# Kernel tuning notes

Measured on AMD Instinct MI355X. Metric: run time of the kernel, lower is better.

The kernel has to match this reference:

```python
import jax, jax.numpy as jnp
import numpy as np

EYE_PENALTY = 1.0e6


def setup_inputs() -> dict:
    key = jax.random.key(0)
    k1, k2 = jax.random.split(key)
    B, NIN, NK, DK = 512, 1024, 128, 5
    x = jax.random.normal(k1, (B, NIN), dtype=jnp.float32)
    theta = jax.random.normal(k2, (NIN, NK, DK), dtype=jnp.float32) * 0.05
    log_weight_scale = jnp.zeros((NK, DK), dtype=jnp.float32)
    bias = jnp.full((NK,), -1.0, dtype=jnp.float32)
    return {"x": x, "theta": theta, "log_weight_scale": log_weight_scale, "bias": bias}


def reference(x, theta, log_weight_scale, bias):
    # kernel = theta * exp(log_weight_scale) / ||theta||_2 (norm over input dim)
    l2 = jnp.sqrt(jnp.sum(theta * theta, axis=0))            # [K, D]
    kernel = theta * (jnp.exp(log_weight_scale) / l2)[None]   # [NIN, K, D]
    actv = jnp.einsum('bi,ikd->bkd', x, kernel)               # [B, K, D]
    B = x.shape[0]
    # all-pairs L1 distance per kernel: [B, K, B]
    diff = actv[:, :, :, None] - jnp.transpose(actv, (1, 2, 0))[None]  # [B,K,D,B]
    abs_dif = jnp.sum(jnp.abs(diff), axis=2)                  # [B, K, B]
    abs_dif = abs_dif + EYE_PENALTY * jnp.eye(B, dtype=x.dtype)[:, None, :]
    f = jnp.sum(jnp.exp(-abs_dif), axis=2) + bias[None, :]    # [B, K]
    return jnp.concatenate([x, f], axis=1)                    # [B, NIN + K]
```

## Files before the change

### kernel.cpp

```cpp
#include <hip/hip_runtime.h>
#include <hip/hip_fp16.h>
#include <math.h>

constexpr int B    = 512;
constexpr int NIN  = 1024;
constexpr int NK   = 128;
constexpr int DK   = 5;
constexpr int NF   = NK * DK;
constexpr int NOUT = NIN + NK;
constexpr int SPLITK = 8;
constexpr int LDA = 136;
#define LOG2E 1.44269504088896f

typedef _Float16 f16x2 __attribute__((ext_vector_type(2)));
typedef _Float16 f16x4 __attribute__((ext_vector_type(4)));
typedef _Float16 f16x8 __attribute__((ext_vector_type(8)));
typedef float    f32x4 __attribute__((ext_vector_type(4)));

union H2 { __half2 h; f16x2 v; unsigned u; };

__global__ __launch_bounds__(256) void gemm_kernel(
        const float* __restrict__ x,
        const float* __restrict__ theta,
        __half* __restrict__ actvP16,
        float* __restrict__ ps) {
    __shared__ _Float16 Ath[64 * LDA];
    __shared__ _Float16 Bxh[64 * LDA];
    __shared__ float    red2[16][64];

    const int t    = threadIdx.x;
    const int tile = blockIdx.x >> 3;
    const int z    = blockIdx.x & 7;
    const int n0   = (tile >> 3) * 64;
    const int b0   = (tile & 7) * 64;
    const bool do_ps = (tile & 7) == 0;
    const int kw   = z * 128;

    const int kq  = t >> 4;
    const int tn4 = (t & 15) * 4;
    float4 tv[8];
    #pragma unroll
    for (int i = 0; i < 8; ++i)
        tv[i] = *(const float4*)&theta[(kw + kq * 8 + i) * NF + n0 + tn4];

    const int br = t >> 2;
    const int ki = t & 3;
    float4 xv[8];
    #pragma unroll
    for (int i = 0; i < 8; ++i)
        xv[i] = *(const float4*)&x[(b0 + br) * NIN + kw + (ki + i * 4) * 4];

    if (do_ps) {
        float sq0 = 0.f, sq1 = 0.f, sq2 = 0.f, sq3 = 0.f;
        #pragma unroll
        for (int i = 0; i < 8; ++i) {
            sq0 += tv[i].x * tv[i].x;  sq1 += tv[i].y * tv[i].y;
            sq2 += tv[i].z * tv[i].z;  sq3 += tv[i].w * tv[i].w;
        }
        red2[kq][tn4 + 0] = sq0;  red2[kq][tn4 + 1] = sq1;
        red2[kq][tn4 + 2] = sq2;  red2[kq][tn4 + 3] = sq3;
    }

    {
        f16x8 h;
        #pragma unroll
        for (int i = 0; i < 8; ++i) h[i] = (_Float16)tv[i].x;
        *(f16x8*)&Ath[(tn4 + 0) * LDA + kq * 8] = h;
        #pragma unroll
        for (int i = 0; i < 8; ++i) h[i] = (_Float16)tv[i].y;
        *(f16x8*)&Ath[(tn4 + 1) * LDA + kq * 8] = h;
        #pragma unroll
        for (int i = 0; i < 8; ++i) h[i] = (_Float16)tv[i].z;
        *(f16x8*)&Ath[(tn4 + 2) * LDA + kq * 8] = h;
        #pragma unroll
        for (int i = 0; i < 8; ++i) h[i] = (_Float16)tv[i].w;
        *(f16x8*)&Ath[(tn4 + 3) * LDA + kq * 8] = h;
    }
    #pragma unroll
    for (int i = 0; i < 8; ++i) {
        f16x4 h;
        h[0] = (_Float16)xv[i].x;  h[1] = (_Float16)xv[i].y;
        h[2] = (_Float16)xv[i].z;  h[3] = (_Float16)xv[i].w;
        *(f16x4*)&Bxh[br * LDA + (ki + i * 4) * 4] = h;
    }
    __syncthreads();

    const int w   = t >> 6;
    const int l   = t & 63;
    const int r16 = l & 15;
    const int kg  = l >> 4;

    f32x4 acc0 = {0.f,0.f,0.f,0.f}, acc1 = {0.f,0.f,0.f,0.f};
    f32x4 acc2 = {0.f,0.f,0.f,0.f}, acc3 = {0.f,0.f,0.f,0.f};
    #pragma unroll
    for (int ks = 0; ks < 4; ++ks) {
        const f16x8 av  = *(const f16x8*)&Ath[(w*16 + r16)*LDA + ks*32 + kg*8];
        const f16x8 bv0 = *(const f16x8*)&Bxh[( 0 + r16)*LDA + ks*32 + kg*8];
        const f16x8 bv1 = *(const f16x8*)&Bxh[(16 + r16)*LDA + ks*32 + kg*8];
        const f16x8 bv2 = *(const f16x8*)&Bxh[(32 + r16)*LDA + ks*32 + kg*8];
        const f16x8 bv3 = *(const f16x8*)&Bxh[(48 + r16)*LDA + ks*32 + kg*8];
        acc0 = __builtin_amdgcn_mfma_f32_16x16x32_f16(av, bv0, acc0, 0, 0, 0);
        acc1 = __builtin_amdgcn_mfma_f32_16x16x32_f16(av, bv1, acc1, 0, 0, 0);
        acc2 = __builtin_amdgcn_mfma_f32_16x16x32_f16(av, bv2, acc2, 0, 0, 0);
        acc3 = __builtin_amdgcn_mfma_f32_16x16x32_f16(av, bv3, acc3, 0, 0, 0);
    }

    {
        __half* dst = actvP16 + (size_t)z * NF * B
                    + (size_t)(n0 + w*16 + kg*4) * B + b0 + r16;
        #pragma unroll
        for (int j = 0; j < 4; ++j) {
            dst[j*B +  0] = __float2half(acc0[j]);
            dst[j*B + 16] = __float2half(acc1[j]);
            dst[j*B + 32] = __float2half(acc2[j]);
            dst[j*B + 48] = __float2half(acc3[j]);
        }
    }
    if (do_ps) {
        __syncthreads();
        if (t < 64) {
            float tot = 0.f;
            #pragma unroll
            for (int rr = 0; rr < 16; ++rr) tot += red2[rr][t];
            ps[z * NF + n0 + t] = tot;
        }
    }
}

__global__ __launch_bounds__(256) void pairwise_kernel(
        const __half* __restrict__ actvP16,
        const float* __restrict__ ps,
        const float* __restrict__ lws,
        const float* __restrict__ bias,
        const float* __restrict__ x,
        float* __restrict__ out) {
    __shared__ __half a16s[DK * B];
    __shared__ float  red[8 * 64];
    __shared__ float  s_sh[DK];
    __shared__ float  red_ps[DK * SPLITK];

    const int k = blockIdx.x;
    const int e = blockIdx.y;
    const int t = threadIdx.x;

    if (e < 4) {
        const int row = k * 4 + e;
        ((float4*)out)[row * (NOUT/4) + t] = ((const float4*)x)[row * (NIN/4) + t];
    }

    if (t < DK * SPLITK)
        red_ps[t] = ps[(t / DK) * NF + k * DK + (t % DK)];

    const size_t slab = (size_t)k * DK * B;
    float acc0f[8], acc1f[8];
    {
        #pragma unroll
        for (int i = 0; i < 8; ++i) { acc0f[i] = 0.f; acc1f[i] = 0.f; }
        #pragma unroll
        for (int z = 0; z < SPLITK; ++z) {
            const f16x8 v = *(const f16x8*)(actvP16 + (size_t)z * NF * B + slab + t * 8);
            #pragma unroll
            for (int i = 0; i < 8; ++i) acc0f[i] += (float)v[i];
        }
        if (t < 64) {
            #pragma unroll
            for (int z = 0; z < SPLITK; ++z) {
                const f16x8 v = *(const f16x8*)(actvP16 + (size_t)z * NF * B + slab + 2048 + t * 8);
                #pragma unroll
                for (int i = 0; i < 8; ++i) acc1f[i] += (float)v[i];
            }
        }
    }
    __syncthreads();
    if (t < DK) {
        float sum = 0.f;
        #pragma unroll
        for (int c = 0; c < SPLITK; ++c) sum += red_ps[c * DK + t];
        s_sh[t] = __expf(lws[k * DK + t]) * rsqrtf(sum) * LOG2E;
    }
    __syncthreads();
    {
        const float s0 = s_sh[t >> 6];
        f16x8 h;
        #pragma unroll
        for (int i = 0; i < 8; ++i) h[i] = (_Float16)(acc0f[i] * s0);
        *(f16x8*)&a16s[t * 8] = h;
        if (t < 64) {
            const float s1 = s_sh[4];
            #pragma unroll
            for (int i = 0; i < 8; ++i) h[i] = (_Float16)(acc1f[i] * s1);
            *(f16x8*)&a16s[2048 + t * 8] = h;
        }
    }
    __syncthreads();

    const int g  = t >> 5;
    const int r  = t & 31;
    const int ba = e * 64 + r;
    const int bb = ba + 32;

    __half2 A2[DK], B2[DK];
    #pragma unroll
    for (int d = 0; d < DK; ++d) {
        A2[d] = __half2half2(a16s[d * B + ba]);
        B2[d] = __half2half2(a16s[d * B + bb]);
    }
    const H2 ones = {__half2half2(__float2half(1.0f))};

    float accA = 0.f, accB = 0.f;
    const int bp0 = g * 64;

    union W8 { f16x8 v; __half2 h[4]; };
    #pragma unroll 2
    for (int m = 0; m < 8; ++m) {
        const int bp = bp0 + m * 8;
        W8 w0, w1, w2, w3, w4;
        w0.v = *(const f16x8*)&a16s[0*B + bp];
        w1.v = *(const f16x8*)&a16s[1*B + bp];
        w2.v = *(const f16x8*)&a16s[2*B + bp];
        w3.v = *(const f16x8*)&a16s[3*B + bp];
        w4.v = *(const f16x8*)&a16s[4*B + bp];
        #pragma unroll
        for (int c = 0; c < 4; ++c) {
            __half2 dA = __habs2(__hsub2(A2[0], w0.h[c]));
            dA = __hadd2(dA, __habs2(__hsub2(A2[1], w1.h[c])));
            dA = __hadd2(dA, __habs2(__hsub2(A2[2], w2.h[c])));
            dA = __hadd2(dA, __habs2(__hsub2(A2[3], w3.h[c])));
            dA = __hadd2(dA, __habs2(__hsub2(A2[4], w4.h[c])));
            H2 eA; eA.h = h2exp2(__hneg2(dA));
            __half2 dB = __habs2(__hsub2(B2[0], w0.h[c]));
            dB = __hadd2(dB, __habs2(__hsub2(B2[1], w1.h[c])));
            dB = __hadd2(dB, __habs2(__hsub2(B2[2], w2.h[c])));
            dB = __hadd2(dB, __habs2(__hsub2(B2[3], w3.h[c])));
            dB = __hadd2(dB, __habs2(__hsub2(B2[4], w4.h[c])));
            H2 eB; eB.h = h2exp2(__hneg2(dB));
#if __has_builtin(__builtin_amdgcn_fdot2)
            accA = __builtin_amdgcn_fdot2(eA.v, ones.v, accA, false);
            accB = __builtin_amdgcn_fdot2(eB.v, ones.v, accB, false);
#else
            accA += __low2float(eA.h) + __high2float(eA.h);
            accB += __low2float(eB.h) + __high2float(eB.h);
#endif
        }
    }
    red[g * 64 + r]      = accA;
    red[g * 64 + 32 + r] = accB;
    __syncthreads();
    if (t < 64) {
        float f = -1.0f + bias[k];
        #pragma unroll
        for (int gg = 0; gg < 8; ++gg) f += red[gg * 64 + t];
        out[(e * 64 + t) * NOUT + NIN + k] = f;
    }
}

extern "C" void kernel_launch(void* const* d_in, const int* in_sizes, int n_in,
                              void* d_out, int out_size, void* d_ws, size_t ws_size,
                              hipStream_t stream) {
    const float* x     = (const float*)d_in[0];
    const float* theta = (const float*)d_in[1];
    const float* lws   = (const float*)d_in[2];
    const float* bias  = (const float*)d_in[3];
    float* out = (float*)d_out;

    char* wsb = (char*)d_ws;
    float*  ps       = (float*)wsb;
    __half* actvP16  = (__half*)(wsb + (64 << 10));

    gemm_kernel<<<dim3(640), 256, 0, stream>>>(x, theta, actvP16, ps);
    pairwise_kernel<<<dim3(NK, 8), 256, 0, stream>>>(actvP16, ps, lws, bias, x, out);
}
```

Before: 24.82 us.

## Halve GEMM N-tile to double blocks; widen pairwise blocks to 512 threads

The GEMM now uses 32-wide feature tiles instead of 64, so it launches twice as many blocks with fewer MFMAs and less theta staging per block. This aims to fill more CUs. The pairwise kernel moves to 512-thread blocks covering 128 query rows, over a grid of NK x 4. Separate thread ranges handle the x copy, the ps load and the split-K reduction, so each slab of activations is reduced and rescaled by half as many blocks. In exchange, the redundant x loads per GEMM block double, and each pairwise block carries more per-block serial work.

```diff
diff --git a/kernel.cpp b/kernel.cpp
--- a/kernel.cpp
+++ b/kernel.cpp
@@ -12,36 +12,37 @@
 constexpr int LDA = 136;
 #define LOG2E 1.44269504088896f
 
-typedef _Float16 f16x2 __attribute__((ext_vector_type(2)));
 typedef _Float16 f16x4 __attribute__((ext_vector_type(4)));
 typedef _Float16 f16x8 __attribute__((ext_vector_type(8)));
 typedef float    f32x4 __attribute__((ext_vector_type(4)));
 
-union H2 { __half2 h; f16x2 v; unsigned u; };
+union H2 { __half2 h; unsigned u; };
 
 __global__ __launch_bounds__(256) void gemm_kernel(
         const float* __restrict__ x,
         const float* __restrict__ theta,
         __half* __restrict__ actvP16,
         float* __restrict__ ps) {
-    __shared__ _Float16 Ath[64 * LDA];
+    __shared__ _Float16 Ath[32 * LDA];
     __shared__ _Float16 Bxh[64 * LDA];
-    __shared__ float    red2[16][64];
+    __shared__ float    red2[32][33];
 
     const int t    = threadIdx.x;
     const int tile = blockIdx.x >> 3;
     const int z    = blockIdx.x & 7;
-    const int n0   = (tile >> 3) * 64;
-    const int b0   = (tile & 7) * 64;
-    const bool do_ps = (tile & 7) == 0;
+    const int nt   = tile >> 3;
+    const int bt   = tile & 7;
+    const int n0   = nt * 32;
+    const int b0   = bt * 64;
+    const bool do_ps = (bt == 0);
     const int kw   = z * 128;
 
-    const int kq  = t >> 4;
-    const int tn4 = (t & 15) * 4;
-    float4 tv[8];
-    #pragma unroll
-    for (int i = 0; i < 8; ++i)
-        tv[i] = *(const float4*)&theta[(kw + kq * 8 + i) * NF + n0 + tn4];
+    const int kq = t >> 3;
+    const int nc = (t & 7) * 4;
+    float4 tv0 = *(const float4*)&theta[(kw + kq*4 + 0) * NF + n0 + nc];
+    float4 tv1 = *(const float4*)&theta[(kw + kq*4 + 1) * NF + n0 + nc];
+    float4 tv2 = *(const float4*)&theta[(kw + kq*4 + 2) * NF + n0 + nc];
+    float4 tv3 = *(const float4*)&theta[(kw + kq*4 + 3) * NF + n0 + nc];
 
     const int br = t >> 2;
     const int ki = t & 3;
@@ -51,30 +52,22 @@
         xv[i] = *(const float4*)&x[(b0 + br) * NIN + kw + (ki + i * 4) * 4];
 
     if (do_ps) {
-        float sq0 = 0.f, sq1 = 0.f, sq2 = 0.f, sq3 = 0.f;
-        #pragma unroll
-        for (int i = 0; i < 8; ++i) {
-            sq0 += tv[i].x * tv[i].x;  sq1 += tv[i].y * tv[i].y;
-            sq2 += tv[i].z * tv[i].z;  sq3 += tv[i].w * tv[i].w;
-        }
-        red2[kq][tn4 + 0] = sq0;  red2[kq][tn4 + 1] = sq1;
-        red2[kq][tn4 + 2] = sq2;  red2[kq][tn4 + 3] = sq3;
+        red2[kq][nc + 0] = tv0.x*tv0.x + tv1.x*tv1.x + tv2.x*tv2.x + tv3.x*tv3.x;
+        red2[kq][nc + 1] = tv0.y*tv0.y + tv1.y*tv1.y + tv2.y*tv2.y + tv3.y*tv3.y;
+        red2[kq][nc + 2] = tv0.z*tv0.z + tv1.z*tv1.z + tv2.z*tv2.z + tv3.z*tv3.z;
+        red2[kq][nc + 3] = tv0.w*tv0.w + tv1.w*tv1.w + tv2.w*tv2.w + tv3.w*tv3.w;
     }
 
     {
-        f16x8 h;
-        #pragma unroll
-        for (int i = 0; i < 8; ++i) h[i] = (_Float16)tv[i].x;
-        *(f16x8*)&Ath[(tn4 + 0) * LDA + kq * 8] = h;
-        #pragma unroll
-        for (int i = 0; i < 8; ++i) h[i] = (_Float16)tv[i].y;
-        *(f16x8*)&Ath[(tn4 + 1) * LDA + kq * 8] = h;
-        #pragma unroll
-        for (int i = 0; i < 8; ++i) h[i] = (_Float16)tv[i].z;
-        *(f16x8*)&Ath[(tn4 + 2) * LDA + kq * 8] = h;
-        #pragma unroll
-        for (int i = 0; i < 8; ++i) h[i] = (_Float16)tv[i].w;
-        *(f16x8*)&Ath[(tn4 + 3) * LDA + kq * 8] = h;
+        f16x4 h;
+        h[0]=(_Float16)tv0.x; h[1]=(_Float16)tv1.x; h[2]=(_Float16)tv2.x; h[3]=(_Float16)tv3.x;
+        *(f16x4*)&Ath[(nc + 0) * LDA + kq * 4] = h;
+        h[0]=(_Float16)tv0.y; h[1]=(_Float16)tv1.y; h[2]=(_Float16)tv2.y; h[3]=(_Float16)tv3.y;
+        *(f16x4*)&Ath[(nc + 1) * LDA + kq * 4] = h;
+        h[0]=(_Float16)tv0.z; h[1]=(_Float16)tv1.z; h[2]=(_Float16)tv2.z; h[3]=(_Float16)tv3.z;
+        *(f16x4*)&Ath[(nc + 2) * LDA + kq * 4] = h;
+        h[0]=(_Float16)tv0.w; h[1]=(_Float16)tv1.w; h[2]=(_Float16)tv2.w; h[3]=(_Float16)tv3.w;
+        *(f16x4*)&Ath[(nc + 3) * LDA + kq * 4] = h;
     }
     #pragma unroll
     for (int i = 0; i < 8; ++i) {
@@ -91,43 +84,36 @@
     const int kg  = l >> 4;
 
     f32x4 acc0 = {0.f,0.f,0.f,0.f}, acc1 = {0.f,0.f,0.f,0.f};
-    f32x4 acc2 = {0.f,0.f,0.f,0.f}, acc3 = {0.f,0.f,0.f,0.f};
     #pragma unroll
     for (int ks = 0; ks < 4; ++ks) {
-        const f16x8 av  = *(const f16x8*)&Ath[(w*16 + r16)*LDA + ks*32 + kg*8];
-        const f16x8 bv0 = *(const f16x8*)&Bxh[( 0 + r16)*LDA + ks*32 + kg*8];
-        const f16x8 bv1 = *(const f16x8*)&Bxh[(16 + r16)*LDA + ks*32 + kg*8];
-        const f16x8 bv2 = *(const f16x8*)&Bxh[(32 + r16)*LDA + ks*32 + kg*8];
-        const f16x8 bv3 = *(const f16x8*)&Bxh[(48 + r16)*LDA + ks*32 + kg*8];
-        acc0 = __builtin_amdgcn_mfma_f32_16x16x32_f16(av, bv0, acc0, 0, 0, 0);
-        acc1 = __builtin_amdgcn_mfma_f32_16x16x32_f16(av, bv1, acc1, 0, 0, 0);
-        acc2 = __builtin_amdgcn_mfma_f32_16x16x32_f16(av, bv2, acc2, 0, 0, 0);
-        acc3 = __builtin_amdgcn_mfma_f32_16x16x32_f16(av, bv3, acc3, 0, 0, 0);
+        const f16x8 bv  = *(const f16x8*)&Bxh[(w*16 + r16)*LDA + ks*32 + kg*8];
+        const f16x8 av0 = *(const f16x8*)&Ath[( 0 + r16)*LDA + ks*32 + kg*8];
+        const f16x8 av1 = *(const f16x8*)&Ath[(16 + r16)*LDA + ks*32 + kg*8];
+        acc0 = __builtin_amdgcn_mfma_f32_16x16x32_f16(av0, bv, acc0, 0, 0, 0);
+        acc1 = __builtin_amdgcn_mfma_f32_16x16x32_f16(av1, bv, acc1, 0, 0, 0);
     }
 
     {
         __half* dst = actvP16 + (size_t)z * NF * B
-                    + (size_t)(n0 + w*16 + kg*4) * B + b0 + r16;
+                    + (size_t)(n0 + kg*4) * B + b0 + w*16 + r16;
         #pragma unroll
         for (int j = 0; j < 4; ++j) {
-            dst[j*B +  0] = __float2half(acc0[j]);
-            dst[j*B + 16] = __float2half(acc1[j]);
-            dst[j*B + 32] = __float2half(acc2[j]);
-            dst[j*B + 48] = __float2half(acc3[j]);
+            dst[j*B]          = __float2half(acc0[j]);
+            dst[(16 + j) * B] = __float2half(acc1[j]);
         }
     }
     if (do_ps) {
         __syncthreads();
-        if (t < 64) {
+        if (t < 32) {
             float tot = 0.f;
             #pragma unroll
-            for (int rr = 0; rr < 16; ++rr) tot += red2[rr][t];
+            for (int rr = 0; rr < 32; ++rr) tot += red2[rr][t];
             ps[z * NF + n0 + t] = tot;
         }
     }
 }
 
-__global__ __launch_bounds__(256) void pairwise_kernel(
+__global__ __launch_bounds__(512) void pairwise_kernel(
         const __half* __restrict__ actvP16,
         const float* __restrict__ ps,
         const float* __restrict__ lws,
@@ -135,7 +121,7 @@
         const float* __restrict__ x,
         float* __restrict__ out) {
     __shared__ __half a16s[DK * B];
-    __shared__ float  red[8 * 64];
+    __shared__ float  red[8 * 128];
     __shared__ float  s_sh[DK];
     __shared__ float  red_ps[DK * SPLITK];
 
@@ -143,32 +129,26 @@
     const int e = blockIdx.y;
     const int t = threadIdx.x;
 
-    if (e < 4) {
+    if (t >= 256) {
+        const int u = t - 256;
         const int row = k * 4 + e;
-        ((float4*)out)[row * (NOUT/4) + t] = ((const float4*)x)[row * (NIN/4) + t];
-    }
-
-    if (t < DK * SPLITK)
-        red_ps[t] = ps[(t / DK) * NF + k * DK + (t % DK)];
+        ((float4*)out)[row * (NOUT/4) + u] = ((const float4*)x)[row * (NIN/4) + u];
+    }
+    if (t >= 448 && t < 448 + DK * SPLITK) {
+        const int u = t - 448;
+        red_ps[u] = ps[(u / DK) * NF + k * DK + (u % DK)];
+    }
 
     const size_t slab = (size_t)k * DK * B;
-    float acc0f[8], acc1f[8];
-    {
-        #pragma unroll
-        for (int i = 0; i < 8; ++i) { acc0f[i] = 0.f; acc1f[i] = 0.f; }
+    float accf[8];
+    #pragma unroll
+    for (int i = 0; i < 8; ++i) accf[i] = 0.f;
+    if (t < 320) {
         #pragma unroll
         for (int z = 0; z < SPLITK; ++z) {
             const f16x8 v = *(const f16x8*)(actvP16 + (size_t)z * NF * B + slab + t * 8);
             #pragma unroll
-            for (int i = 0; i < 8; ++i) acc0f[i] += (float)v[i];
-        }
-        if (t < 64) {
-            #pragma unroll
-            for (int z = 0; z < SPLITK; ++z) {
-                const f16x8 v = *(const f16x8*)(actvP16 + (size_t)z * NF * B + slab + 2048 + t * 8);
-                #pragma unroll
-                for (int i = 0; i < 8; ++i) acc1f[i] += (float)v[i];
-            }
+            for (int i = 0; i < 8; ++i) accf[i] += (float)v[i];
         }
     }
     __syncthreads();
@@ -179,25 +159,19 @@
         s_sh[t] = __expf(lws[k * DK + t]) * rsqrtf(sum) * LOG2E;
     }
     __syncthreads();
-    {
-        const float s0 = s_sh[t >> 6];
+    if (t < 320) {
+        const float s = s_sh[t >> 6];
         f16x8 h;
         #pragma unroll
-        for (int i = 0; i < 8; ++i) h[i] = (_Float16)(acc0f[i] * s0);
+        for (int i = 0; i < 8; ++i) h[i] = (_Float16)(accf[i] * s);
         *(f16x8*)&a16s[t * 8] = h;
-        if (t < 64) {
-            const float s1 = s_sh[4];
-            #pragma unroll
-            for (int i = 0; i < 8; ++i) h[i] = (_Float16)(acc1f[i] * s1);
-            *(f16x8*)&a16s[2048 + t * 8] = h;
-        }
-    }
-    __syncthreads();
-
-    const int g  = t >> 5;
-    const int r  = t & 31;
-    const int ba = e * 64 + r;
-    const int bb = ba + 32;
+    }
+    __syncthreads();
+
+    const int g  = t >> 6;
+    const int r  = t & 63;
+    const int ba = e * 128 + r;
+    const int bb = ba + 64;
 
     __half2 A2[DK], B2[DK];
     #pragma unroll
@@ -205,12 +179,15 @@
         A2[d] = __half2half2(a16s[d * B + ba]);
         B2[d] = __half2half2(a16s[d * B + bb]);
     }
-    const H2 ones = {__half2half2(__float2half(1.0f))};
 
     float accA = 0.f, accB = 0.f;
     const int bp0 = g * 64;
 
     union W8 { f16x8 v; __half2 h[4]; };
+    typedef _Float16 f16x2v __attribute__((ext_vector_type(2)));
+    union HV { __half2 h; f16x2v v; };
+    const HV ones = {__half2half2(__float2half(1.0f))};
+
     #pragma unroll 2
     for (int m = 0; m < 8; ++m) {
         const int bp = bp0 + m * 8;
@@ -227,13 +204,13 @@
             dA = __hadd2(dA, __habs2(__hsub2(A2[2], w2.h[c])));
             dA = __hadd2(dA, __habs2(__hsub2(A2[3], w3.h[c])));
             dA = __hadd2(dA, __habs2(__hsub2(A2[4], w4.h[c])));
-            H2 eA; eA.h = h2exp2(__hneg2(dA));
+            HV eA; eA.h = h2exp2(__hneg2(dA));
             __half2 dB = __habs2(__hsub2(B2[0], w0.h[c]));
             dB = __hadd2(dB, __habs2(__hsub2(B2[1], w1.h[c])));
             dB = __hadd2(dB, __habs2(__hsub2(B2[2], w2.h[c])));
             dB = __hadd2(dB, __habs2(__hsub2(B2[3], w3.h[c])));
             dB = __hadd2(dB, __habs2(__hsub2(B2[4], w4.h[c])));
-            H2 eB; eB.h = h2exp2(__hneg2(dB));
+            HV eB; eB.h = h2exp2(__hneg2(dB));
 #if __has_builtin(__builtin_amdgcn_fdot2)
             accA = __builtin_amdgcn_fdot2(eA.v, ones.v, accA, false);
             accB = __builtin_amdgcn_fdot2(eB.v, ones.v, accB, false);
@@ -243,14 +220,14 @@
 #endif
         }
     }
-    red[g * 64 + r]      = accA;
-    red[g * 64 + 32 + r] = accB;
-    __syncthreads();
-    if (t < 64) {
+    red[g * 128 + r]      = accA;
+    red[g * 128 + 64 + r] = accB;
+    __syncthreads();
+    if (t < 128) {
         float f = -1.0f + bias[k];
         #pragma unroll
-        for (int gg = 0; gg < 8; ++gg) f += red[gg * 64 + t];
-        out[(e * 64 + t) * NOUT + NIN + k] = f;
+        for (int gg = 0; gg < 8; ++gg) f += red[gg * 128 + t];
+        out[(e * 128 + t) * NOUT + NIN + k] = f;
     }
 }
 
@@ -267,6 +244,6 @@
     float*  ps       = (float*)wsb;
     __half* actvP16  = (__half*)(wsb + (64 << 10));
 
-    gemm_kernel<<<dim3(640), 256, 0, stream>>>(x, theta, actvP16, ps);
-    pairwise_kernel<<<dim3(NK, 8), 256, 0, stream>>>(actvP16, ps, lws, bias, x, out);
+    gemm_kernel<<<dim3(1280), 256, 0, stream>>>(x, theta, actvP16, ps);
+    pairwise_kernel<<<dim3(NK, 4), 512, 0, stream>>>(actvP16, ps, lws, bias, x, out);
 }
```

Measured after the change: 24.00 us. -3.3%, faster.
